# Optimization experiments

Measured on AMD Instinct MI355X. Metric: run time of the kernel, lower is better.

The kernel has to match this reference:

```python
import jax, jax.numpy as jnp
import numpy as np

HEADS = 4
C_HEAD = 32


def setup_inputs() -> dict:
    key = jax.random.key(0)
    k1, k2, k3 = jax.random.split(key, 3)
    c_in = 256
    c_hid = HEADS * C_HEAD  # 128
    x = jax.random.normal(k1, (4, c_in, 64, 64), dtype=jnp.float32)
    # 1x1 conv weights stored as [out, in]
    w_qkv = jax.random.normal(k2, (3 * c_hid, c_in), dtype=jnp.float32) * (c_in ** -0.5)
    w_out = jax.random.normal(k3, (c_in, c_hid), dtype=jnp.float32) * (c_hid ** -0.5)
    b_out = jnp.zeros((c_in,), dtype=jnp.float32)
    return {"x": x, "w_qkv": w_qkv, "w_out": w_out, "b_out": b_out}


def reference(x, w_qkv, w_out, b_out):
    b, c, h, w = x.shape
    scale = C_HEAD ** -0.5
    # 1x1 conv == channel matmul
    qkv = jnp.einsum('bchw,oc->bohw', x, w_qkv)  # [b, 3*c_hid, h, w]
    q, k, v = jnp.split(qkv, 3, axis=1)
    # b (heads c_head) x y -> b heads c_head (x y)
    def to_heads(t):
        return t.reshape(b, HEADS, C_HEAD, h * w)
    q, k, v = to_heads(q) * scale, to_heads(k), to_heads(v)
    sim = jnp.einsum('bhci,bhcj->bhij', q, k)  # [b, heads, N, N]
    sim = sim - jax.lax.stop_gradient(jnp.max(sim, axis=-1, keepdims=True))
    attn = jax.nn.softmax(sim, axis=-1)
    out = jnp.einsum('bhij,bhcj->bhic', attn, v)  # [b, heads, N, c_head]
    # b h (x y) c -> b (h c) x y
    out = out.transpose(0, 1, 3, 2).reshape(b, HEADS * C_HEAD, h, w)
    out = jnp.einsum('bchw,oc->bohw', out, w_out) + b_out[None, :, None, None]
    return out
```

## Files before the change

### kernel.cpp

```cpp
#include <hip/hip_runtime.h>
#include <hip/hip_bf16.h>
#include <cstdint>
#include <cstddef>


#define NB 4
#define CIN 256
#define CHID 128
#define HEADS 4
#define CHEAD 32
#define NPOS 4096
#define BH 16
#define NTOT 16384
#define QKV_O 384
#define QSCALE_LOG2E 0.2550348229f

typedef float f32x2 __attribute__((ext_vector_type(2)));
typedef float f32x4 __attribute__((ext_vector_type(4)));
typedef float f32x16 __attribute__((ext_vector_type(16)));
typedef short s16x8 __attribute__((ext_vector_type(8)));

static __device__ __forceinline__ unsigned short f2bf(float f) {
    union { float f; unsigned u; } v; v.f = f;
    unsigned r = v.u + 0x7FFFu + ((v.u >> 16) & 1u);
    return (unsigned short)(r >> 16);
}

static __device__ __forceinline__ unsigned int pk2bf(float a, float b) {
    union { __hip_bfloat162 h; unsigned int u; } c;
    c.h = __float22bfloat162_rn(float2{a, b});
    return c.u;
}

static __device__ __forceinline__ void plswap(unsigned& a, unsigned& b) {
#if __has_builtin(__builtin_amdgcn_permlane32_swap)
    auto r = __builtin_amdgcn_permlane32_swap((int)a, (int)b, false, false);
    a = (unsigned)r[0];
    b = (unsigned)r[1];
#else
    int hh = (threadIdx.x >> 5) & 1;
    unsigned ta = (unsigned)__shfl_xor((int)a, 32);
    unsigned tb = (unsigned)__shfl_xor((int)b, 32);
    unsigned na = hh ? tb : a;
    unsigned nb = hh ? b : ta;
    a = na; b = nb;
#endif
}

static __device__ __forceinline__ s16x8 mk8(unsigned a, unsigned b, unsigned c, unsigned d) {
    union { unsigned u[4]; s16x8 v; } x;
    x.u[0] = a; x.u[1] = b; x.u[2] = c; x.u[3] = d;
    return x.v;
}

static __device__ __forceinline__ void async_cp16(const void* g, void* l) {
    __builtin_amdgcn_global_load_lds((const __attribute__((address_space(1))) unsigned int*)g,
                                     (__attribute__((address_space(3))) unsigned int*)l, 16, 0, 0);
}

#define MFMA32(a, b, c) __builtin_amdgcn_mfma_f32_32x32x16_bf16(a, b, c, 0, 0, 0)

#define TBLOCKS (NB * (CIN / 32) * (NPOS / 32))
__global__ __launch_bounds__(256) void k_prep(const float* __restrict__ x,
                                              unsigned short* __restrict__ xT,
                                              const float* __restrict__ wqkv,
                                              const float* __restrict__ wout,
                                              unsigned short* __restrict__ wqkv_bf,
                                              unsigned short* __restrict__ wout_bf) {
    if (blockIdx.x >= TBLOCKS) {
        int i = (blockIdx.x - TBLOCKS) * 256 + threadIdx.x;
        if (i < QKV_O * CIN) wqkv_bf[i] = f2bf(wqkv[i]);
        if (i < CIN * CHID)  wout_bf[i] = f2bf(wout[i]);
        return;
    }
    __shared__ float tile[32][33];
    const int ntiles = NPOS / 32;
    const int ctiles = CIN / 32;
    int b   = blockIdx.x / (ntiles * ctiles);
    int rem = blockIdx.x % (ntiles * ctiles);
    int ct = rem / ntiles;
    int nt = rem % ntiles;
    int c0 = ct * 32, n0 = nt * 32;
    int tc = threadIdx.x / 32;
    int tn = threadIdx.x % 32;
    const float* xb = x + (size_t)b * CIN * NPOS;
#pragma unroll
    for (int it = 0; it < 4; ++it) {
        int c = tc + it * 8;
        tile[c][tn] = xb[(size_t)(c0 + c) * NPOS + n0 + tn];
    }
    __syncthreads();
    unsigned short* xTb = xT + (size_t)b * NPOS * CIN;
#pragma unroll
    for (int it = 0; it < 4; ++it) {
        int n = tc + it * 8;
        xTb[(size_t)(n0 + n) * CIN + c0 + tn] = f2bf(tile[tn][n]);
    }
}

__global__ __launch_bounds__(256, 4) void k_qkv(const unsigned short* __restrict__ wq,
                                                const unsigned short* __restrict__ xT,
                                                unsigned short* __restrict__ Q,
                                                unsigned short* __restrict__ K,
                                                unsigned short* __restrict__ V) {
    __shared__ __align__(16) unsigned char smem[2 * 12288];
    int mt = blockIdx.x % 3;
    int nt = blockIdx.x / 3;
    int wid = threadIdx.x >> 6, lane = threadIdx.x & 63;
    int quad = lane >> 4, low4 = lane & 15;
    int o0 = mt * 128, n0 = nt * 64;
    int lb = lane * 16;

    const unsigned short* srcA0 = wq + (size_t)(o0 + wid * 32 + low4) * CIN + quad * 8;
    const unsigned short* srcA1 = srcA0 + 16 * CIN;
    const unsigned short* srcB  = xT + (size_t)(n0 + wid * 16 + low4) * CIN + quad * 8;
    int dA0 = wid * 2048, dA1 = dA0 + 1024, dB = 8192 + wid * 1024;

    async_cp16(srcA0, smem + dA0 + lb);
    async_cp16(srcA1, smem + dA1 + lb);
    async_cp16(srcB,  smem + dB  + lb);
    __syncthreads();

    f32x4 acc[2][4] = {};
    for (int c = 0; c < 8; ++c) {
        if (c < 7) {
            unsigned char* nxt = smem + ((c + 1) & 1) * 12288;
            async_cp16(srcA0 + (c + 1) * 32, nxt + dA0 + lb);
            async_cp16(srcA1 + (c + 1) * 32, nxt + dA1 + lb);
            async_cp16(srcB  + (c + 1) * 32, nxt + dB  + lb);
        }
        const unsigned char* cur = smem + (c & 1) * 12288;
        s16x8 a0 = *(const s16x8*)(cur + wid * 2048 + lb);
        s16x8 a1 = *(const s16x8*)(cur + wid * 2048 + 1024 + lb);
#pragma unroll
        for (int j = 0; j < 4; ++j) {
            s16x8 bj = *(const s16x8*)(cur + 8192 + j * 1024 + lb);
            acc[0][j] = __builtin_amdgcn_mfma_f32_16x16x32_bf16(a0, bj, acc[0][j], 0, 0, 0);
            acc[1][j] = __builtin_amdgcn_mfma_f32_16x16x32_bf16(a1, bj, acc[1][j], 0, 0, 0);
        }
        __syncthreads();
    }

    if (mt < 2) {
        unsigned short* dst = (mt == 0) ? Q : K;
        float sc = (mt == 0) ? QSCALE_LOG2E : 1.0f;
#pragma unroll
        for (int i = 0; i < 2; ++i) {
            int ol = wid * 32 + i * 16 + quad * 4;
            int head = ol >> 5, ch = ol & 31;
#pragma unroll
            for (int j = 0; j < 4; ++j) {
                int nG = n0 + j * 16 + low4;
                int b = nG >> 12, n = nG & 4095;
                f32x4 v = acc[i][j];
                unsigned long long d =
                    (unsigned long long)pk2bf(v[0] * sc, v[1] * sc) |
                    ((unsigned long long)pk2bf(v[2] * sc, v[3] * sc) << 32);
                *(unsigned long long*)(dst + ((size_t)(b * 4 + head) * NPOS + n) * 32 + ch) = d;
            }
        }
    } else {
        unsigned short* vt = (unsigned short*)smem;
#pragma unroll
        for (int i = 0; i < 2; ++i) {
            int ol = wid * 32 + i * 16 + quad * 4;
#pragma unroll
            for (int j = 0; j < 4; ++j) {
                int col = j * 16 + low4;
#pragma unroll
                for (int r = 0; r < 4; ++r) vt[(ol + r) * 80 + col] = f2bf(acc[i][j][r]);
            }
        }
        __syncthreads();
        int b = n0 >> 12, nbase = n0 & 4095;
#pragma unroll
        for (int rep = 0; rep < 4; ++rep) {
            int idx = rep * 256 + threadIdx.x;
            int row = idx >> 3, c8 = idx & 7;
            s16x8 val = *(const s16x8*)(vt + row * 80 + c8 * 8);
            int head = row >> 5, ch = row & 31;
            *(s16x8*)(V + ((size_t)((b * 4 + head) * 32 + ch)) * NPOS + nbase + c8 * 8) = val;
        }
    }
}

__global__ __launch_bounds__(256, 4) void k_attn(const unsigned short* __restrict__ Q,
                                                 const unsigned short* __restrict__ K,
                                                 const unsigned short* __restrict__ V,
                                                 unsigned short* __restrict__ attnO) {
    __shared__ __align__(16) unsigned char smem[2 * 16384];
    int bh = blockIdx.x & 15;
    int qt = blockIdx.x >> 4;
    int wid = threadIdx.x >> 6;
    int lane = threadIdx.x & 63;
    int q5 = lane & 31, h = lane >> 5;
    int qg = wid & 1, kh = wid >> 1;
    int q0 = qt * 64 + qg * 32;
    int khk = kh * 2048;

    const unsigned short* Qp  = Q + (size_t)bh * NPOS * 32;
    const unsigned short* Kbh = K + (size_t)bh * NPOS * 32;
    const unsigned short* Vbh = V + (size_t)bh * 32 * NPOS;

    s16x8 bq0 = *(const s16x8*)(Qp + (size_t)(q0 + q5) * 32 + h * 8);
    s16x8 bq1 = *(const s16x8*)(Qp + (size_t)(q0 + q5) * 32 + 16 + h * 8);

    const unsigned short* sK = Kbh + (size_t)q5 * 32 + h * 8;
    const unsigned short* sV = Vbh + (size_t)q5 * NPOS + h * 8;

    auto stage = [&](int bufi, int k0) {
        unsigned char* wb = smem + bufi * 16384 + kh * 8192;
        if (qg == 0) {
            const unsigned short* p = sK + (size_t)k0 * 32;
            async_cp16(p,        wb);
            async_cp16(p + 16,   wb + 1024);
            async_cp16(p + 1024, wb + 2048);
            async_cp16(p + 1040, wb + 3072);
        } else {
            const unsigned short* p = sV + k0;
            async_cp16(p,      wb + 4096);
            async_cp16(p + 16, wb + 5120);
            async_cp16(p + 32, wb + 6144);
            async_cp16(p + 48, wb + 7168);
        }
    };

    f32x16 oT = {};
    f32x2 lacc0 = {0.0f, 0.0f}, lacc1 = {0.0f, 0.0f};
    const int lby = lane * 16;

    auto softmax_tile = [&](const f32x16& s, s16x8& bplo, s16x8& bphi) {
        unsigned p[8];
#pragma unroll
        for (int i = 0; i < 8; ++i) {
            float e0 = __builtin_amdgcn_exp2f(s[2 * i]);
            float e1 = __builtin_amdgcn_exp2f(s[2 * i + 1]);
            f32x2 e = {e0, e1};
            if (i & 1) lacc0 += e;
            else       lacc1 += e;
            p[i] = pk2bf(e0, e1);
        }
        plswap(p[0], p[2]); plswap(p[1], p[3]);
        plswap(p[4], p[6]); plswap(p[5], p[7]);
        bplo = mk8(p[0], p[1], p[2], p[3]);
        bphi = mk8(p[4], p[5], p[6], p[7]);
    };

    stage(0, khk);
    __syncthreads();

#pragma unroll 1
    for (int it = 0; it < 32; ++it) {
        const unsigned char* kb = smem + (it & 1) * 16384 + kh * 8192;
        s16x8 ak00 = *(const s16x8*)(kb + lby);
        s16x8 ak01 = *(const s16x8*)(kb + 1024 + lby);
        s16x8 ak10 = *(const s16x8*)(kb + 2048 + lby);
        s16x8 ak11 = *(const s16x8*)(kb + 3072 + lby);
        s16x8 av00 = *(const s16x8*)(kb + 4096 + lby);
        s16x8 av01 = *(const s16x8*)(kb + 5120 + lby);
        s16x8 av10 = *(const s16x8*)(kb + 6144 + lby);
        s16x8 av11 = *(const s16x8*)(kb + 7168 + lby);
        if (it + 1 < 32) stage((it + 1) & 1, khk + (it + 1) * 64);
        __syncthreads();

        f32x16 s0 = {};
        s0 = MFMA32(ak00, bq0, s0);
        s0 = MFMA32(ak01, bq1, s0);
        s16x8 bplo0, bphi0;
        softmax_tile(s0, bplo0, bphi0);
        f32x16 s1 = {};
        s1 = MFMA32(ak10, bq0, s1);
        s1 = MFMA32(ak11, bq1, s1);
        oT = MFMA32(av00, bplo0, oT);
        oT = MFMA32(av01, bphi0, oT);
        s16x8 bplo1, bphi1;
        softmax_tile(s1, bplo1, bphi1);
        oT = MFMA32(av10, bplo1, oT);
        oT = MFMA32(av11, bphi1, oT);
    }

    float lsum = lacc0[0] + lacc0[1] + lacc1[0] + lacc1[1];
    lsum += __shfl_xor(lsum, 32);

    if (kh) {
        float* area = (float*)(smem + qg * 4352);
#pragma unroll
        for (int j = 0; j < 4; ++j)
            *(f32x4*)(area + j * 256 + lane * 4) =
                f32x4{oT[4 * j], oT[4 * j + 1], oT[4 * j + 2], oT[4 * j + 3]};
        area[1024 + lane] = lsum;
    }
    __syncthreads();
    if (!kh) {
        const float* area = (const float*)(smem + qg * 4352);
        lsum += area[1024 + lane];
        float inv = 1.0f / lsum;
        int b = bh >> 2, head = bh & 3;
        int n = q0 + q5;
        unsigned short* base = attnO + ((size_t)(b * NPOS + n)) * CHID + head * 32 + 4 * h;
#pragma unroll
        for (int j = 0; j < 4; ++j) {
            f32x4 r = *(const f32x4*)(area + j * 256 + lane * 4);
            unsigned long long d =
                (unsigned long long)pk2bf((oT[4 * j] + r[0]) * inv, (oT[4 * j + 1] + r[1]) * inv) |
                ((unsigned long long)pk2bf((oT[4 * j + 2] + r[2]) * inv, (oT[4 * j + 3] + r[3]) * inv) << 32);
            *(unsigned long long*)(base + 8 * j) = d;
        }
    }
}

__global__ __launch_bounds__(256, 4) void k_out(const unsigned short* __restrict__ wo,
                                                const unsigned short* __restrict__ attnO,
                                                const float* __restrict__ bias,
                                                float* __restrict__ out) {
    __shared__ __align__(16) unsigned char smem[2 * 12288];
    int mt = blockIdx.x & 1;
    int nt = blockIdx.x >> 1;
    int wid = threadIdx.x >> 6, lane = threadIdx.x & 63;
    int quad = lane >> 4, low4 = lane & 15;
    int o0 = mt * 128, n0 = nt * 64;
    int lb = lane * 16;

    const unsigned short* srcA0 = wo + (size_t)(o0 + wid * 32 + low4) * CHID + quad * 8;
    const unsigned short* srcA1 = srcA0 + 16 * CHID;
    const unsigned short* srcB  = attnO + (size_t)(n0 + wid * 16 + low4) * CHID + quad * 8;
    int dA0 = wid * 2048, dA1 = dA0 + 1024, dB = 8192 + wid * 1024;

    async_cp16(srcA0, smem + dA0 + lb);
    async_cp16(srcA1, smem + dA1 + lb);
    async_cp16(srcB,  smem + dB  + lb);
    __syncthreads();

    f32x4 acc[2][4] = {};
    for (int c = 0; c < 4; ++c) {
        if (c < 3) {
            unsigned char* nxt = smem + ((c + 1) & 1) * 12288;
            async_cp16(srcA0 + (c + 1) * 32, nxt + dA0 + lb);
            async_cp16(srcA1 + (c + 1) * 32, nxt + dA1 + lb);
            async_cp16(srcB  + (c + 1) * 32, nxt + dB  + lb);
        }
        const unsigned char* cur = smem + (c & 1) * 12288;
        s16x8 a0 = *(const s16x8*)(cur + wid * 2048 + lb);
        s16x8 a1 = *(const s16x8*)(cur + wid * 2048 + 1024 + lb);
#pragma unroll
        for (int j = 0; j < 4; ++j) {
            s16x8 bj = *(const s16x8*)(cur + 8192 + j * 1024 + lb);
            acc[0][j] = __builtin_amdgcn_mfma_f32_16x16x32_bf16(a0, bj, acc[0][j], 0, 0, 0);
            acc[1][j] = __builtin_amdgcn_mfma_f32_16x16x32_bf16(a1, bj, acc[1][j], 0, 0, 0);
        }
        __syncthreads();
    }

#pragma unroll
    for (int i = 0; i < 2; ++i) {
        int ob = o0 + wid * 32 + i * 16 + quad * 4;
#pragma unroll
        for (int j = 0; j < 4; ++j) {
            int nG = n0 + j * 16 + low4;
            int b = nG >> 12, n = nG & 4095;
#pragma unroll
            for (int r = 0; r < 4; ++r) {
                int o = ob + r;
                out[((size_t)(b * CIN + o)) * NPOS + n] = acc[i][j][r] + bias[o];
            }
        }
    }
}

extern "C" void kernel_launch(void* const* d_in, const int* in_sizes, int n_in,
                              void* d_out, int out_size, void* d_ws, size_t ws_size,
                              hipStream_t stream) {
    const float* x    = (const float*)d_in[0];
    const float* wqkv = (const float*)d_in[1];
    const float* wout = (const float*)d_in[2];
    const float* bout = (const float*)d_in[3];
    float* out = (float*)d_out;

    unsigned short* Q       = (unsigned short*)d_ws;
    unsigned short* K       = Q + (size_t)BH * NPOS * 32;
    unsigned short* V       = K + (size_t)BH * NPOS * 32;
    unsigned short* attnO   = V + (size_t)BH * 32 * NPOS;
    unsigned short* xT      = attnO + (size_t)NTOT * CHID;
    unsigned short* wqkv_bf = xT + (size_t)NTOT * CIN;
    unsigned short* wout_bf = wqkv_bf + QKV_O * CIN;

    k_prep<<<TBLOCKS + (QKV_O * CIN + 255) / 256, 256, 0, stream>>>(x, xT, wqkv, wout, wqkv_bf, wout_bf);
    k_qkv<<<3 * (NTOT / 64), 256, 0, stream>>>(wqkv_bf, xT, Q, K, V);
    k_attn<<<(NPOS / 64) * BH, 256, 0, stream>>>(Q, K, V, attnO);
    k_out<<<2 * (NTOT / 64), 256, 0, stream>>>(wout_bf, attnO, bout, out);
}
```

Measured before the change: 158.8 us.

## Load K/V tiles directly into registers with software prefetch instead of LDS staging

Replaces the double-buffered async global-to-LDS staging of K and V tiles, and its per-iteration block barrier, with direct global loads into registers. Next-iteration tiles are prefetched mid-loop. Shared memory shrinks to the reduction area only, which may raise occupancy. In exchange, the two wave pairs that used to share each staged tile now both load the same K/V data from global/L2, which doubles that traffic and adds register pressure. The last iteration also issues one wrapped-around, redundant prefetch.

```diff
diff --git a/kernel.cpp b/kernel.cpp
--- a/kernel.cpp
+++ b/kernel.cpp
@@ -188,7 +188,7 @@
                                                  const unsigned short* __restrict__ K,
                                                  const unsigned short* __restrict__ V,
                                                  unsigned short* __restrict__ attnO) {
-    __shared__ __align__(16) unsigned char smem[2 * 16384];
+    __shared__ __align__(16) unsigned char smem[8704];
     int bh = blockIdx.x & 15;
     int qt = blockIdx.x >> 4;
     int wid = threadIdx.x >> 6;
@@ -205,29 +205,14 @@
     s16x8 bq0 = *(const s16x8*)(Qp + (size_t)(q0 + q5) * 32 + h * 8);
     s16x8 bq1 = *(const s16x8*)(Qp + (size_t)(q0 + q5) * 32 + 16 + h * 8);
 
-    const unsigned short* sK = Kbh + (size_t)q5 * 32 + h * 8;
-    const unsigned short* sV = Vbh + (size_t)q5 * NPOS + h * 8;
-
-    auto stage = [&](int bufi, int k0) {
-        unsigned char* wb = smem + bufi * 16384 + kh * 8192;
-        if (qg == 0) {
-            const unsigned short* p = sK + (size_t)k0 * 32;
-            async_cp16(p,        wb);
-            async_cp16(p + 16,   wb + 1024);
-            async_cp16(p + 1024, wb + 2048);
-            async_cp16(p + 1040, wb + 3072);
-        } else {
-            const unsigned short* p = sV + k0;
-            async_cp16(p,      wb + 4096);
-            async_cp16(p + 16, wb + 5120);
-            async_cp16(p + 32, wb + 6144);
-            async_cp16(p + 48, wb + 7168);
-        }
-    };
+    const unsigned short* pK = Kbh + (size_t)q5 * 32 + h * 8;
+    const unsigned short* pV = Vbh + (size_t)q5 * NPOS + h * 8;
+
+#define LK(k0, t, f) (*(const s16x8*)(pK + (size_t)(k0) * 32 + (t) * 1024 + (f) * 16))
+#define LV(k0, c)    (*(const s16x8*)(pV + (k0) + (c) * 16))
 
     f32x16 oT = {};
     f32x2 lacc0 = {0.0f, 0.0f}, lacc1 = {0.0f, 0.0f};
-    const int lby = lane * 16;
 
     auto softmax_tile = [&](const f32x16& s, s16x8& bplo, s16x8& bphi) {
         unsigned p[8];
@@ -246,38 +231,45 @@
         bphi = mk8(p[4], p[5], p[6], p[7]);
     };
 
-    stage(0, khk);
-    __syncthreads();
+    s16x8 ak00 = LK(khk, 0, 0), ak01 = LK(khk, 0, 1);
+    s16x8 ak10 = LK(khk, 1, 0), ak11 = LK(khk, 1, 1);
+    s16x8 av00 = LV(khk, 0), av01 = LV(khk, 1);
+    s16x8 av10 = LV(khk, 2), av11 = LV(khk, 3);
 
 #pragma unroll 1
     for (int it = 0; it < 32; ++it) {
-        const unsigned char* kb = smem + (it & 1) * 16384 + kh * 8192;
-        s16x8 ak00 = *(const s16x8*)(kb + lby);
-        s16x8 ak01 = *(const s16x8*)(kb + 1024 + lby);
-        s16x8 ak10 = *(const s16x8*)(kb + 2048 + lby);
-        s16x8 ak11 = *(const s16x8*)(kb + 3072 + lby);
-        s16x8 av00 = *(const s16x8*)(kb + 4096 + lby);
-        s16x8 av01 = *(const s16x8*)(kb + 5120 + lby);
-        s16x8 av10 = *(const s16x8*)(kb + 6144 + lby);
-        s16x8 av11 = *(const s16x8*)(kb + 7168 + lby);
-        if (it + 1 < 32) stage((it + 1) & 1, khk + (it + 1) * 64);
-        __syncthreads();
+        int k0n = khk + ((it + 1) & 31) * 64;
 
         f32x16 s0 = {};
         s0 = MFMA32(ak00, bq0, s0);
         s0 = MFMA32(ak01, bq1, s0);
         s16x8 bplo0, bphi0;
         softmax_tile(s0, bplo0, bphi0);
+
         f32x16 s1 = {};
         s1 = MFMA32(ak10, bq0, s1);
         s1 = MFMA32(ak11, bq1, s1);
+
+        s16x8 nk00 = LK(k0n, 0, 0), nk01 = LK(k0n, 0, 1);
+        s16x8 nk10 = LK(k0n, 1, 0), nk11 = LK(k0n, 1, 1);
+
         oT = MFMA32(av00, bplo0, oT);
         oT = MFMA32(av01, bphi0, oT);
+
         s16x8 bplo1, bphi1;
         softmax_tile(s1, bplo1, bphi1);
+
         oT = MFMA32(av10, bplo1, oT);
         oT = MFMA32(av11, bphi1, oT);
-    }
+
+        s16x8 nv00 = LV(k0n, 0), nv01 = LV(k0n, 1);
+        s16x8 nv10 = LV(k0n, 2), nv11 = LV(k0n, 3);
+
+        ak00 = nk00; ak01 = nk01; ak10 = nk10; ak11 = nk11;
+        av00 = nv00; av01 = nv01; av10 = nv10; av11 = nv11;
+    }
+#undef LK
+#undef LV
 
     float lsum = lacc0[0] + lacc0[1] + lacc1[0] + lacc1[1];
     lsum += __shfl_xor(lsum, 32);
```

Result: slower. 181.4 us (+14.2%).
